# Kernel optimization log

Measured on AMD Instinct MI355X. Metric: run time of the kernel, lower is better.

Reference implementation:

```python
import jax, jax.numpy as jnp
import numpy as np

EMBED = 1024
HEADS = 16
B, T = 4, 2048


def setup_inputs() -> dict:
    key = jax.random.key(0)
    k1, k2, k3, k4, k5 = jax.random.split(key, 5)
    s = 1.0 / np.sqrt(EMBED)
    x = jax.random.normal(k1, (B, T, EMBED), dtype=jnp.float32)
    w_attn = jax.random.uniform(k2, (3 * EMBED, EMBED), dtype=jnp.float32, minval=-s, maxval=s)
    b_attn = jax.random.uniform(k3, (3 * EMBED,), dtype=jnp.float32, minval=-s, maxval=s)
    w_proj = jax.random.uniform(k4, (EMBED, EMBED), dtype=jnp.float32, minval=-s, maxval=s)
    b_proj = jax.random.uniform(k5, (EMBED,), dtype=jnp.float32, minval=-s, maxval=s)
    return {"x": x, "w_attn": w_attn, "b_attn": b_attn, "w_proj": w_proj, "b_proj": b_proj}


def reference(x, w_attn, b_attn, w_proj, b_proj):
    Bn, Tn, C = x.shape
    nh = HEADS
    hs = C // nh
    # fused QKV projection: (B,T,C) @ (C,3C) + b
    qkv = jnp.einsum('btc,fc->btf', x, w_attn) + b_attn
    q, k, v = jnp.split(qkv, 3, axis=-1)
    # split heads -> (B, nh, T, hs)
    q = q.reshape(Bn, Tn, nh, hs).transpose(0, 2, 1, 3)
    k = k.reshape(Bn, Tn, nh, hs).transpose(0, 2, 1, 3)
    v = v.reshape(Bn, Tn, nh, hs).transpose(0, 2, 1, 3)
    scale = 1.0 / jnp.sqrt(jnp.asarray(hs, dtype=x.dtype))
    att = jnp.einsum('bhqd,bhkd->bhqk', q, k) * scale  # (B, nh, T, T)
    causal_mask = jnp.tril(jnp.ones((Tn, Tn), dtype=bool))
    att = jnp.where(causal_mask, att, jnp.asarray(-jnp.inf, dtype=att.dtype))
    att = jax.nn.softmax(att, axis=-1)
    y = jnp.einsum('bhqk,bhkd->bhqd', att, v)  # (B, nh, T, hs)
    y = y.transpose(0, 2, 1, 3).reshape(Bn, Tn, C)
    # output projection (dropout=0 in eval mode -> identity)
    y = jnp.einsum('btc,oc->bto', y, w_proj) + b_proj
    return y
```

## Files before the change

### kernel.cpp

```cpp
#include <hip/hip_runtime.h>
#include <hip/hip_bf16.h>
#include <stdint.h>

typedef __bf16 bf16_t;
typedef __bf16 bf16x8 __attribute__((ext_vector_type(8)));
typedef __bf16 bf16x4 __attribute__((ext_vector_type(4)));
typedef float f32x4 __attribute__((ext_vector_type(4)));

#define AS1 __attribute__((address_space(1)))
#define AS3 __attribute__((address_space(3)))

static __device__ __forceinline__ void gload_lds16(const void* g, void* l) {
  __builtin_amdgcn_global_load_lds((const AS1 void*)g, (AS3 void*)l, 16, 0, 0);
}

static __device__ __forceinline__ uint32_t cvt_pk(float lo, float hi) {
  uint32_t r;
  asm("v_cvt_pk_bf16_f32 %0, %1, %2" : "=v"(r) : "v"(lo), "v"(hi));
  return r;
}

__global__ void cvt_f32_bf16(const float* __restrict__ in, bf16_t* __restrict__ out, int n4) {
  int i = blockIdx.x * blockDim.x + threadIdx.x;
  if (i >= n4) return;
  float4 v = ((const float4*)in)[i];
  bf16x4 o;
  o[0] = (bf16_t)v.x; o[1] = (bf16_t)v.y; o[2] = (bf16_t)v.z; o[3] = (bf16_t)v.w;
  *(bf16x4*)(out + (size_t)i * 4) = o;
}

template<int MODE>
__global__ __launch_bounds__(256) void gemm_bt(
    const bf16_t* __restrict__ A, const bf16_t* __restrict__ Bw,
    const float* __restrict__ bias, void* __restrict__ Cout,
    int M, int N, int K)
{
  __shared__ bf16_t As[128 * 32];
  __shared__ bf16_t Bs[128 * 32];
  const int tid = threadIdx.x;
  const int wave = tid >> 6, lane = tid & 63;
  const int l15 = lane & 15, l4 = lane >> 4;
  const int nwgx = gridDim.x;
  const int fid = blockIdx.y * nwgx + blockIdx.x;
  const int qq = (nwgx * gridDim.y) >> 3;
  const int nid = (fid & 7) * qq + (fid >> 3);
  const int m0 = (nid / nwgx) * 128, n0 = (nid % nwgx) * 128;
  const int wm = (wave >> 1) * 64, wn = (wave & 1) * 64;
  f32x4 acc[4][4] = {};

  const int r = tid >> 2;
  const int cb = (tid & 3) * 16;
  const char* gA0 = (const char*)(A + (size_t)(m0 + r) * K) + cb;
  const char* gA1 = (const char*)(A + (size_t)(m0 + 64 + r) * K) + cb;
  const char* gB0 = (const char*)(Bw + (size_t)(n0 + r) * K) + cb;
  const char* gB1 = (const char*)(Bw + (size_t)(n0 + 64 + r) * K) + cb;
  char* lA = (char*)As + tid * 16;
  char* lB = (char*)Bs + tid * 16;

  for (int k0 = 0; k0 < K; k0 += 32) {
    const size_t koff = (size_t)k0 * 2;
    gload_lds16(gA0 + koff, lA);
    gload_lds16(gA1 + koff, lA + 4096);
    gload_lds16(gB0 + koff, lB);
    gload_lds16(gB1 + koff, lB + 4096);
    __syncthreads();
    bf16x8 af[4], bfr[4];
#pragma unroll
    for (int mt = 0; mt < 4; ++mt)
      af[mt] = *(const bf16x8*)&As[(wm + mt * 16 + l15) * 32 + l4 * 8];
#pragma unroll
    for (int nt = 0; nt < 4; ++nt)
      bfr[nt] = *(const bf16x8*)&Bs[(wn + nt * 16 + l15) * 32 + l4 * 8];
#pragma unroll
    for (int mt = 0; mt < 4; ++mt)
#pragma unroll
      for (int nt = 0; nt < 4; ++nt)
        acc[mt][nt] = __builtin_amdgcn_mfma_f32_16x16x32_bf16(af[mt], bfr[nt], acc[mt][nt], 0, 0, 0);
    __syncthreads();
  }

  if (MODE == 0) {
    bf16_t* qkv = (bf16_t*)Cout;
#pragma unroll
    for (int mt = 0; mt < 4; ++mt) {
#pragma unroll
      for (int nt = 0; nt < 4; ++nt) {
        const int col = n0 + wn + nt * 16 + l15;
        const float bv = bias[col];
        const int which = col >> 10;
        const int c = col & 1023;
        const int head = c >> 6, d = c & 63;
#pragma unroll
        for (int i = 0; i < 4; ++i) {
          const int row = m0 + wm + mt * 16 + l4 * 4 + i;
          const int bb = row >> 11, t = row & 2047;
          const int bh2 = bb * 16 + head;
          float v = acc[mt][nt][i] + bv;
          size_t idx;
          if (which == 0) {
            v *= 0.125f;
            idx = ((size_t)(bh2 * 2048 + t) << 6) + d;
          } else if (which == 1) {
            idx = 8388608 + ((size_t)(bh2 * 2048 + t) << 6) + d;
          } else {
            const int ko = t & 63;
            const int pos = (ko & 0x20) | ((ko & 0x0C) << 1) | ((ko & 0x10) >> 2) | (ko & 3);
            idx = 16777216 + (size_t)bh2 * 131072 + ((size_t)(t >> 6) << 12) + d * 64 + pos;
          }
          qkv[idx] = (bf16_t)v;
        }
      }
    }
  } else {
    float* C = (float*)Cout;
#pragma unroll
    for (int mt = 0; mt < 4; ++mt) {
#pragma unroll
      for (int nt = 0; nt < 4; ++nt) {
        const int col = n0 + wn + nt * 16 + l15;
        const float bv = bias[col];
#pragma unroll
        for (int i = 0; i < 4; ++i) {
          const int row = m0 + wm + mt * 16 + l4 * 4 + i;
          C[(size_t)row * N + col] = acc[mt][nt][i] + bv;
        }
      }
    }
  }
}

static __device__ __forceinline__ void half_step(
    const bf16x8& kA0, const bf16x8& kB0, const bf16x8& kA1, const bf16x8& kB1,
    const bf16x8& kA2, const bf16x8& kB2, const bf16x8& kA3, const bf16x8& kB3,
    const bf16x8& vA0, const bf16x8& vB0, const bf16x8& vA1, const bf16x8& vB1,
    const bf16x8& vA2, const bf16x8& vB2, const bf16x8& vA3, const bf16x8& vB3,
    const bf16x8 aq0, const bf16x8 aq1,
    float& m_i, float& l_i,
    f32x4& o0, f32x4& o1, f32x4& o2, f32x4& o3,
    const bool diag, const int qb, const int kb)
{
  f32x4 s0 = {}, s1 = {}, s2 = {}, s3 = {};
  s0 = __builtin_amdgcn_mfma_f32_16x16x32_bf16(kA0, aq0, s0, 0, 0, 0);
  s0 = __builtin_amdgcn_mfma_f32_16x16x32_bf16(kB0, aq1, s0, 0, 0, 0);
  s1 = __builtin_amdgcn_mfma_f32_16x16x32_bf16(kA1, aq0, s1, 0, 0, 0);
  s1 = __builtin_amdgcn_mfma_f32_16x16x32_bf16(kB1, aq1, s1, 0, 0, 0);
  s2 = __builtin_amdgcn_mfma_f32_16x16x32_bf16(kA2, aq0, s2, 0, 0, 0);
  s2 = __builtin_amdgcn_mfma_f32_16x16x32_bf16(kB2, aq1, s2, 0, 0, 0);
  s3 = __builtin_amdgcn_mfma_f32_16x16x32_bf16(kA3, aq0, s3, 0, 0, 0);
  s3 = __builtin_amdgcn_mfma_f32_16x16x32_bf16(kB3, aq1, s3, 0, 0, 0);

  if (diag) {
#pragma unroll
    for (int i = 0; i < 4; ++i) {
      if (kb + i > qb)      s0[i] = -1e30f;
      if (16 + kb + i > qb) s1[i] = -1e30f;
      if (32 + kb + i > qb) s2[i] = -1e30f;
      if (48 + kb + i > qb) s3[i] = -1e30f;
    }
  }

  float pm = fmaxf(fmaxf(fmaxf(s0[0], s0[1]), fmaxf(s0[2], s0[3])),
                   fmaxf(fmaxf(s1[0], s1[1]), fmaxf(s1[2], s1[3])));
  pm = fmaxf(pm, fmaxf(fmaxf(fmaxf(s2[0], s2[1]), fmaxf(s2[2], s2[3])),
                       fmaxf(fmaxf(s3[0], s3[1]), fmaxf(s3[2], s3[3]))));
  pm = fmaxf(pm, __shfl_xor(pm, 16));
  pm = fmaxf(pm, __shfl_xor(pm, 32));

  const bool keep = __all(pm - m_i <= 8.f);
  const float mn = keep ? m_i : fmaxf(m_i, pm);
  const float sc = keep ? 1.f : __expf(m_i - mn);
  m_i = mn;
#pragma unroll
  for (int i = 0; i < 4; ++i) {
    s0[i] = __expf(s0[i] - mn);
    s1[i] = __expf(s1[i] - mn);
    s2[i] = __expf(s2[i] - mn);
    s3[i] = __expf(s3[i] - mn);
  }
  float rs = ((s0[0] + s0[1]) + (s0[2] + s0[3])) + ((s1[0] + s1[1]) + (s1[2] + s1[3]))
           + ((s2[0] + s2[1]) + (s2[2] + s2[3])) + ((s3[0] + s3[1]) + (s3[2] + s3[3]));
  rs += __shfl_xor(rs, 16);
  rs += __shfl_xor(rs, 32);
  if (keep) {
    l_i = l_i + rs;
  } else {
    l_i = l_i * sc + rs;
    o0 *= sc; o1 *= sc; o2 *= sc; o3 *= sc;
  }

  union { uint32_t u[4]; bf16x8 v; } B0, B1;
  B0.u[0] = cvt_pk(s0[0], s0[1]); B0.u[1] = cvt_pk(s0[2], s0[3]);
  B0.u[2] = cvt_pk(s1[0], s1[1]); B0.u[3] = cvt_pk(s1[2], s1[3]);
  B1.u[0] = cvt_pk(s2[0], s2[1]); B1.u[1] = cvt_pk(s2[2], s2[3]);
  B1.u[2] = cvt_pk(s3[0], s3[1]); B1.u[3] = cvt_pk(s3[2], s3[3]);

  o0 = __builtin_amdgcn_mfma_f32_16x16x32_bf16(vA0, B0.v, o0, 0, 0, 0);
  o0 = __builtin_amdgcn_mfma_f32_16x16x32_bf16(vB0, B1.v, o0, 0, 0, 0);
  o1 = __builtin_amdgcn_mfma_f32_16x16x32_bf16(vA1, B0.v, o1, 0, 0, 0);
  o1 = __builtin_amdgcn_mfma_f32_16x16x32_bf16(vB1, B1.v, o1, 0, 0, 0);
  o2 = __builtin_amdgcn_mfma_f32_16x16x32_bf16(vA2, B0.v, o2, 0, 0, 0);
  o2 = __builtin_amdgcn_mfma_f32_16x16x32_bf16(vB2, B1.v, o2, 0, 0, 0);
  o3 = __builtin_amdgcn_mfma_f32_16x16x32_bf16(vA3, B0.v, o3, 0, 0, 0);
  o3 = __builtin_amdgcn_mfma_f32_16x16x32_bf16(vB3, B1.v, o3, 0, 0, 0);
}

__global__ __launch_bounds__(64) void flash_attn(
    const bf16_t* __restrict__ Qg, const bf16_t* __restrict__ Kg,
    const bf16_t* __restrict__ VTg, bf16_t* __restrict__ Y)
{
  const int T = 2048, HS = 64;
  const int flat = blockIdx.x;
  const int xcd = flat & 7;
  const int rest = flat >> 3;
  const int bh = xcd * 8 + (rest & 7);
  const int s = 31 - (rest >> 3);
  const size_t baseQ = (size_t)bh * T * HS;
  const size_t baseV = (size_t)bh * HS * T;

  const int lane = threadIdx.x & 63;
  const int l15 = lane & 15, l4 = lane >> 4;

  const int bound = s;
  const int kb = l4 * 4;
  const int qb0 = l15;
  const int qb1 = l15 + 16;
  const int qb2 = l15 + 32;
  const int qb3 = l15 + 48;

  const bf16_t* qr = Qg + baseQ + (size_t)(64 * s + l15) * HS;
  const bf16x8 aq00 = *(const bf16x8*)(qr + l4 * 8);
  const bf16x8 aq01 = *(const bf16x8*)(qr + 32 + l4 * 8);
  const bf16x8 aq10 = *(const bf16x8*)(qr + 16 * HS + l4 * 8);
  const bf16x8 aq11 = *(const bf16x8*)(qr + 16 * HS + 32 + l4 * 8);
  const bf16x8 aq20 = *(const bf16x8*)(qr + 32 * HS + l4 * 8);
  const bf16x8 aq21 = *(const bf16x8*)(qr + 32 * HS + 32 + l4 * 8);
  const bf16x8 aq30 = *(const bf16x8*)(qr + 48 * HS + l4 * 8);
  const bf16x8 aq31 = *(const bf16x8*)(qr + 48 * HS + 32 + l4 * 8);

  float m0 = -1e30f, l0 = 0.f, m1 = -1e30f, l1 = 0.f;
  float m2 = -1e30f, l2 = 0.f, m3 = -1e30f, l3 = 0.f;
  f32x4 o00 = {}, o01 = {}, o02 = {}, o03 = {};
  f32x4 o10 = {}, o11 = {}, o12 = {}, o13 = {};
  f32x4 o20 = {}, o21 = {}, o22 = {}, o23 = {};
  f32x4 o30 = {}, o31 = {}, o32 = {}, o33 = {};

  const bf16_t* kp = Kg + baseQ + (size_t)l15 * HS + l4 * 8;
  const bf16_t* vp = VTg + baseV + (size_t)l15 * 64 + l4 * 8;

  for (int kt = 0; kt <= bound; ++kt) {
    const bool dg = (kt == bound);
    const bf16x8 kA0 = *(const bf16x8*)(kp + 0);
    const bf16x8 kB0 = *(const bf16x8*)(kp + 32);
    const bf16x8 kA1 = *(const bf16x8*)(kp + 1024);
    const bf16x8 kB1 = *(const bf16x8*)(kp + 1024 + 32);
    const bf16x8 kA2 = *(const bf16x8*)(kp + 2048);
    const bf16x8 kB2 = *(const bf16x8*)(kp + 2048 + 32);
    const bf16x8 kA3 = *(const bf16x8*)(kp + 3072);
    const bf16x8 kB3 = *(const bf16x8*)(kp + 3072 + 32);
    const bf16x8 vA0 = *(const bf16x8*)(vp + 0);
    const bf16x8 vB0 = *(const bf16x8*)(vp + 32);
    const bf16x8 vA1 = *(const bf16x8*)(vp + 1024);
    const bf16x8 vB1 = *(const bf16x8*)(vp + 1024 + 32);
    const bf16x8 vA2 = *(const bf16x8*)(vp + 2048);
    const bf16x8 vB2 = *(const bf16x8*)(vp + 2048 + 32);
    const bf16x8 vA3 = *(const bf16x8*)(vp + 3072);
    const bf16x8 vB3 = *(const bf16x8*)(vp + 3072 + 32);

    half_step(kA0, kB0, kA1, kB1, kA2, kB2, kA3, kB3,
              vA0, vB0, vA1, vB1, vA2, vB2, vA3, vB3,
              aq00, aq01, m0, l0, o00, o01, o02, o03, dg, qb0, kb);
    half_step(kA0, kB0, kA1, kB1, kA2, kB2, kA3, kB3,
              vA0, vB0, vA1, vB1, vA2, vB2, vA3, vB3,
              aq10, aq11, m1, l1, o10, o11, o12, o13, dg, qb1, kb);
    half_step(kA0, kB0, kA1, kB1, kA2, kB2, kA3, kB3,
              vA0, vB0, vA1, vB1, vA2, vB2, vA3, vB3,
              aq20, aq21, m2, l2, o20, o21, o22, o23, dg, qb2, kb);
    half_step(kA0, kB0, kA1, kB1, kA2, kB2, kA3, kB3,
              vA0, vB0, vA1, vB1, vA2, vB2, vA3, vB3,
              aq30, aq31, m3, l3, o30, o31, o32, o33, dg, qb3, kb);

    kp += 4096;
    vp += 4096;
  }

  const int b = bh >> 4, h = bh & 15;
  {
    const float il = 1.f / l0;
    const int q = 64 * s + l15;
    bf16_t* yr = Y + ((size_t)(b * T + q)) * 1024 + h * 64 + l4 * 4;
    uint2 w;
    w.x = cvt_pk(o00[0] * il, o00[1] * il); w.y = cvt_pk(o00[2] * il, o00[3] * il);
    *(uint2*)(yr + 0) = w;
    w.x = cvt_pk(o01[0] * il, o01[1] * il); w.y = cvt_pk(o01[2] * il, o01[3] * il);
    *(uint2*)(yr + 16) = w;
    w.x = cvt_pk(o02[0] * il, o02[1] * il); w.y = cvt_pk(o02[2] * il, o02[3] * il);
    *(uint2*)(yr + 32) = w;
    w.x = cvt_pk(o03[0] * il, o03[1] * il); w.y = cvt_pk(o03[2] * il, o03[3] * il);
    *(uint2*)(yr + 48) = w;
  }
  {
    const float il = 1.f / l1;
    const int q = 64 * s + 16 + l15;
    bf16_t* yr = Y + ((size_t)(b * T + q)) * 1024 + h * 64 + l4 * 4;
    uint2 w;
    w.x = cvt_pk(o10[0] * il, o10[1] * il); w.y = cvt_pk(o10[2] * il, o10[3] * il);
    *(uint2*)(yr + 0) = w;
    w.x = cvt_pk(o11[0] * il, o11[1] * il); w.y = cvt_pk(o11[2] * il, o11[3] * il);
    *(uint2*)(yr + 16) = w;
    w.x = cvt_pk(o12[0] * il, o12[1] * il); w.y = cvt_pk(o12[2] * il, o12[3] * il);
    *(uint2*)(yr + 32) = w;
    w.x = cvt_pk(o13[0] * il, o13[1] * il); w.y = cvt_pk(o13[2] * il, o13[3] * il);
    *(uint2*)(yr + 48) = w;
  }
  {
    const float il = 1.f / l2;
    const int q = 64 * s + 32 + l15;
    bf16_t* yr = Y + ((size_t)(b * T + q)) * 1024 + h * 64 + l4 * 4;
    uint2 w;
    w.x = cvt_pk(o20[0] * il, o20[1] * il); w.y = cvt_pk(o20[2] * il, o20[3] * il);
    *(uint2*)(yr + 0) = w;
    w.x = cvt_pk(o21[0] * il, o21[1] * il); w.y = cvt_pk(o21[2] * il, o21[3] * il);
    *(uint2*)(yr + 16) = w;
    w.x = cvt_pk(o22[0] * il, o22[1] * il); w.y = cvt_pk(o22[2] * il, o22[3] * il);
    *(uint2*)(yr + 32) = w;
    w.x = cvt_pk(o23[0] * il, o23[1] * il); w.y = cvt_pk(o23[2] * il, o23[3] * il);
    *(uint2*)(yr + 48) = w;
  }
  {
    const float il = 1.f / l3;
    const int q = 64 * s + 48 + l15;
    bf16_t* yr = Y + ((size_t)(b * T + q)) * 1024 + h * 64 + l4 * 4;
    uint2 w;
    w.x = cvt_pk(o30[0] * il, o30[1] * il); w.y = cvt_pk(o30[2] * il, o30[3] * il);
    *(uint2*)(yr + 0) = w;
    w.x = cvt_pk(o31[0] * il, o31[1] * il); w.y = cvt_pk(o31[2] * il, o31[3] * il);
    *(uint2*)(yr + 16) = w;
    w.x = cvt_pk(o32[0] * il, o32[1] * il); w.y = cvt_pk(o32[2] * il, o32[3] * il);
    *(uint2*)(yr + 32) = w;
    w.x = cvt_pk(o33[0] * il, o33[1] * il); w.y = cvt_pk(o33[2] * il, o33[3] * il);
    *(uint2*)(yr + 48) = w;
  }
}

extern "C" void kernel_launch(void* const* d_in, const int* in_sizes, int n_in,
                              void* d_out, int out_size, void* d_ws, size_t ws_size,
                              hipStream_t stream) {
  const float* x      = (const float*)d_in[0];
  const float* w_attn = (const float*)d_in[1];
  const float* b_attn = (const float*)d_in[2];
  const float* w_proj = (const float*)d_in[3];
  const float* b_proj = (const float*)d_in[4];
  float* out = (float*)d_out;

  char* ws = (char*)d_ws;
  bf16_t* xb   = (bf16_t*)(ws);
  bf16_t* wab  = (bf16_t*)(ws + 16777216);
  bf16_t* wpb  = (bf16_t*)(ws + 23068672);
  bf16_t* qkvb = (bf16_t*)(ws + 25165824);
  bf16_t* yb   = (bf16_t*)(ws + 75497472);

  cvt_f32_bf16<<<8192, 256, 0, stream>>>(x, xb, 2097152);
  cvt_f32_bf16<<<3072, 256, 0, stream>>>(w_attn, wab, 786432);
  cvt_f32_bf16<<<1024, 256, 0, stream>>>(w_proj, wpb, 262144);

  dim3 g1(24, 64);
  gemm_bt<0><<<g1, 256, 0, stream>>>(xb, wab, b_attn, (void*)qkvb, 8192, 3072, 1024);

  flash_attn<<<2048, 64, 0, stream>>>(qkvb, qkvb + 8388608, qkvb + 16777216, yb);

  dim3 g3(8, 64);
  gemm_bt<1><<<g3, 256, 0, stream>>>(yb, wpb, b_proj, (void*)out, 8192, 1024, 1024);
}
```

Measured before the change: 224.5 us.

## Double GEMM K-tile to 64 with XOR-swizzled LDS and vectorized V epilogue

```diff
diff --git a/kernel.cpp b/kernel.cpp
--- a/kernel.cpp
+++ b/kernel.cpp
@@ -35,8 +35,8 @@
     const float* __restrict__ bias, void* __restrict__ Cout,
     int M, int N, int K)
 {
-  __shared__ bf16_t As[128 * 32];
-  __shared__ bf16_t Bs[128 * 32];
+  __shared__ bf16_t As[128 * 64];
+  __shared__ bf16_t Bs[128 * 64];
   const int tid = threadIdx.x;
   const int wave = tid >> 6, lane = tid & 63;
   const int l15 = lane & 15, l4 = lane >> 4;
@@ -48,29 +48,51 @@
   const int wm = (wave >> 1) * 64, wn = (wave & 1) * 64;
   f32x4 acc[4][4] = {};
 
-  const int r = tid >> 2;
-  const int cb = (tid & 3) * 16;
-  const char* gA0 = (const char*)(A + (size_t)(m0 + r) * K) + cb;
-  const char* gA1 = (const char*)(A + (size_t)(m0 + 64 + r) * K) + cb;
-  const char* gB0 = (const char*)(Bw + (size_t)(n0 + r) * K) + cb;
-  const char* gB1 = (const char*)(Bw + (size_t)(n0 + 64 + r) * K) + cb;
+  const int srow = tid >> 3;
+  const int schunk = ((tid & 7) ^ ((tid >> 3) & 7)) * 8;
+  const bf16_t* gA = A + (size_t)(m0 + srow) * K + schunk;
+  const bf16_t* gB = Bw + (size_t)(n0 + srow) * K + schunk;
   char* lA = (char*)As + tid * 16;
   char* lB = (char*)Bs + tid * 16;
 
-  for (int k0 = 0; k0 < K; k0 += 32) {
-    const size_t koff = (size_t)k0 * 2;
-    gload_lds16(gA0 + koff, lA);
-    gload_lds16(gA1 + koff, lA + 4096);
-    gload_lds16(gB0 + koff, lB);
-    gload_lds16(gB1 + koff, lB + 4096);
+  for (int k0 = 0; k0 < K; k0 += 64) {
+    const bf16_t* ga = gA + k0;
+    const bf16_t* gb = gB + k0;
+    gload_lds16(ga,           lA);
+    gload_lds16(ga + 32 * K,  lA + 4096);
+    gload_lds16(ga + 64 * K,  lA + 8192);
+    gload_lds16(ga + 96 * K,  lA + 12288);
+    gload_lds16(gb,           lB);
+    gload_lds16(gb + 32 * K,  lB + 4096);
+    gload_lds16(gb + 64 * K,  lB + 8192);
+    gload_lds16(gb + 96 * K,  lB + 12288);
     __syncthreads();
     bf16x8 af[4], bfr[4];
 #pragma unroll
+    for (int mt = 0; mt < 4; ++mt) {
+      const int rr = wm + mt * 16 + l15;
+      af[mt] = *(const bf16x8*)((const char*)As + rr * 128 + ((l4 ^ (rr & 7)) << 4));
+    }
+#pragma unroll
+    for (int nt = 0; nt < 4; ++nt) {
+      const int rr = wn + nt * 16 + l15;
+      bfr[nt] = *(const bf16x8*)((const char*)Bs + rr * 128 + ((l4 ^ (rr & 7)) << 4));
+    }
+#pragma unroll
     for (int mt = 0; mt < 4; ++mt)
-      af[mt] = *(const bf16x8*)&As[(wm + mt * 16 + l15) * 32 + l4 * 8];
-#pragma unroll
-    for (int nt = 0; nt < 4; ++nt)
-      bfr[nt] = *(const bf16x8*)&Bs[(wn + nt * 16 + l15) * 32 + l4 * 8];
+#pragma unroll
+      for (int nt = 0; nt < 4; ++nt)
+        acc[mt][nt] = __builtin_amdgcn_mfma_f32_16x16x32_bf16(af[mt], bfr[nt], acc[mt][nt], 0, 0, 0);
+#pragma unroll
+    for (int mt = 0; mt < 4; ++mt) {
+      const int rr = wm + mt * 16 + l15;
+      af[mt] = *(const bf16x8*)((const char*)As + rr * 128 + (((l4 + 4) ^ (rr & 7)) << 4));
+    }
+#pragma unroll
+    for (int nt = 0; nt < 4; ++nt) {
+      const int rr = wn + nt * 16 + l15;
+      bfr[nt] = *(const bf16x8*)((const char*)Bs + rr * 128 + (((l4 + 4) ^ (rr & 7)) << 4));
+    }
 #pragma unroll
     for (int mt = 0; mt < 4; ++mt)
 #pragma unroll
@@ -81,33 +103,53 @@
 
   if (MODE == 0) {
     bf16_t* qkv = (bf16_t*)Cout;
-#pragma unroll
-    for (int mt = 0; mt < 4; ++mt) {
-#pragma unroll
-      for (int nt = 0; nt < 4; ++nt) {
-        const int col = n0 + wn + nt * 16 + l15;
-        const float bv = bias[col];
-        const int which = col >> 10;
-        const int c = col & 1023;
-        const int head = c >> 6, d = c & 63;
-#pragma unroll
-        for (int i = 0; i < 4; ++i) {
-          const int row = m0 + wm + mt * 16 + l4 * 4 + i;
-          const int bb = row >> 11, t = row & 2047;
+    const int which = n0 >> 10;
+    if (which == 2) {
+#pragma unroll
+      for (int mt = 0; mt < 4; ++mt) {
+        const int rb = m0 + wm + mt * 16 + l4 * 4;
+        const int bb = rb >> 11, t = rb & 2047;
+        const int ko = t & 63;
+        const int pos = (ko & 0x20) | ((ko & 0x0C) << 1) | ((ko & 0x10) >> 2);
+        const size_t tilebase = 16777216 + ((size_t)(t >> 6) << 12) + pos;
+#pragma unroll
+        for (int nt = 0; nt < 4; ++nt) {
+          const int col = n0 + wn + nt * 16 + l15;
+          const float bv = bias[col];
+          const int c = col & 1023;
+          const int head = c >> 6, d = c & 63;
           const int bh2 = bb * 16 + head;
-          float v = acc[mt][nt][i] + bv;
-          size_t idx;
-          if (which == 0) {
-            v *= 0.125f;
-            idx = ((size_t)(bh2 * 2048 + t) << 6) + d;
-          } else if (which == 1) {
-            idx = 8388608 + ((size_t)(bh2 * 2048 + t) << 6) + d;
-          } else {
-            const int ko = t & 63;
-            const int pos = (ko & 0x20) | ((ko & 0x0C) << 1) | ((ko & 0x10) >> 2) | (ko & 3);
-            idx = 16777216 + (size_t)bh2 * 131072 + ((size_t)(t >> 6) << 12) + d * 64 + pos;
+          const size_t idx = tilebase + (size_t)bh2 * 131072 + d * 64;
+          uint2 w;
+          w.x = cvt_pk(acc[mt][nt][0] + bv, acc[mt][nt][1] + bv);
+          w.y = cvt_pk(acc[mt][nt][2] + bv, acc[mt][nt][3] + bv);
+          *(uint2*)&qkv[idx] = w;
+        }
+      }
+    } else {
+#pragma unroll
+      for (int mt = 0; mt < 4; ++mt) {
+#pragma unroll
+        for (int nt = 0; nt < 4; ++nt) {
+          const int col = n0 + wn + nt * 16 + l15;
+          const float bv = bias[col];
+          const int c = col & 1023;
+          const int head = c >> 6, d = c & 63;
+#pragma unroll
+          for (int i = 0; i < 4; ++i) {
+            const int row = m0 + wm + mt * 16 + l4 * 4 + i;
+            const int bb = row >> 11, t = row & 2047;
+            const int bh2 = bb * 16 + head;
+            float v = acc[mt][nt][i] + bv;
+            size_t idx;
+            if (which == 0) {
+              v *= 0.125f;
+              idx = ((size_t)(bh2 * 2048 + t) << 6) + d;
+            } else {
+              idx = 8388608 + ((size_t)(bh2 * 2048 + t) << 6) + d;
+            }
+            qkv[idx] = (bf16_t)v;
           }
-          qkv[idx] = (bf16_t)v;
         }
       }
     }
```

Measured after the change: 201.7 us. 10.2% less time.
